# Kernel tuning notes

Hardware: AMD Instinct MI355X
Metric: run time of the kernel (lower is better)

Reference implementation:

```python
import jax, jax.numpy as jnp
import numpy as np

BS, T, N = 16, 50, 100
OBS, ACT, HID, LAT = 40, 8, 64, 16
NEG = -9e15


def _gat(x, adj, w, a_src, a_dst, b, concat, alpha=0.2):
    # x: [B, n, fin]; w: [H, fin, fout]
    h = jnp.einsum('bni,hio->bhno', x, w)
    e_src = jnp.einsum('bhno,ho->bhn', h, a_src[..., 0])
    e_dst = jnp.einsum('bhno,ho->bhn', h, a_dst[..., 0])
    e = e_src[:, :, :, None] + e_dst[:, :, None, :]        # [B,H,n,n]
    e = jnp.where(e > 0, e, alpha * e)                     # LeakyReLU
    e = jnp.where(adj[None, None] > 0, e, NEG)             # mask by adjacency
    att = jax.nn.softmax(e, axis=-1)
    hp = jnp.einsum('bhnm,bhmo->bhno', att, h)
    if concat:
        B, H, n, fo = hp.shape
        return jax.nn.elu(hp.transpose(0, 2, 1, 3).reshape(B, n, H * fo) + b)
    return hp.mean(axis=1) + b


def _lstm(x, Wih, Whh, bih, bhh):
    # x: [B, T, H]; PyTorch gate order i, f, g, o
    def step(carry, xt):
        h, c = carry
        g = xt @ Wih + h @ Whh + bih + bhh
        i, f, gg, o = jnp.split(g, 4, axis=-1)
        c = jax.nn.sigmoid(f) * c + jax.nn.sigmoid(i) * jnp.tanh(gg)
        h = jax.nn.sigmoid(o) * jnp.tanh(c)
        return (h, c), h
    h0 = jnp.zeros((x.shape[0], Whh.shape[0]), x.dtype)
    _, ys = jax.lax.scan(step, (h0, h0), x.transpose(1, 0, 2))
    return ys.transpose(1, 0, 2)


def _forward(o, a_prev, m, eps, params, adj):
    (W_obs, b_obs, W_pa, b_pa, W_mk, b_mk, id_emb,
     lWih, lWhh, lbih, lbhh,
     e1w, e1s, e1d, e1b, e2w, e2s, e2d, e2b,
     d1w, d1s, d1d, d1b, d2w, d2s, d2d, d2b,
     d3w, d3s, d3d, d3b) = params
    bs, t, n, _ = o.shape
    # encode: summed embeddings (dropout is identity in eval)
    emb = (o @ W_obs + b_obs) + (a_prev @ W_pa + b_pa) + (m @ W_mk + b_mk) + id_emb[None, None]
    x = emb.transpose(0, 2, 1, 3).reshape(bs * n, t, HID)
    x = _lstm(x, lWih, lWhh, lbih, lbhh)
    x = x.reshape(bs, n, t, HID).transpose(0, 2, 1, 3).reshape(bs * t, n, HID)
    x = _gat(x, adj, e1w, e1s, e1d, e1b, True)
    x = _gat(x, adj, e2w, e2s, e2d, e2b, False)
    logits = x.reshape(bs, t, n, 2 * LAT).mean(axis=-2)    # AverageGlobalPool over nodes
    mu, logvar = jnp.split(logits, 2, axis=-1)
    z = mu + eps * jnp.exp(0.5 * logvar)                   # reparameterize
    zu = jnp.repeat(z[:, :, None, :], n, axis=2)           # RepeatGlobalUnpool
    d = jnp.concatenate([emb, zu], axis=-1).reshape(bs * t, n, HID + LAT)
    d = _gat(d, adj, d1w, d1s, d1d, d1b, True)
    d = _gat(d, adj, d2w, d2s, d2d, d2b, True)
    d = _gat(d, adj, d3w, d3s, d3d, d3b, False)
    a_recon = d.reshape(bs, t, n, ACT) * m
    return a_recon, mu, logvar


def setup_inputs() -> dict:
    key = jax.random.key(0)
    it = iter(jax.random.split(key, 48))
    def nrm(shape, s=0.1):
        return s * jax.random.normal(next(it), shape, jnp.float32)
    inp = {}
    inp['o'] = jax.random.normal(next(it), (BS, T, N, OBS), jnp.float32)
    inp['a_prev'] = jax.random.uniform(next(it), (BS, T, N, ACT), jnp.float32)
    inp['m'] = (jax.random.uniform(next(it), (BS, T, N, ACT)) > 0.5).astype(jnp.float32)
    inp['eps'] = jax.random.normal(next(it), (BS, T, LAT), jnp.float32)
    adj = jax.random.randint(next(it), (N, N), 0, 2).astype(jnp.int32)
    inp['adj'] = adj.at[jnp.arange(N), jnp.arange(N)].set(1)
    inp['W_obs'] = nrm((OBS, HID)); inp['b_obs'] = jnp.zeros((HID,), jnp.float32)
    inp['W_pa'] = nrm((ACT, HID)); inp['b_pa'] = jnp.zeros((HID,), jnp.float32)
    inp['W_mk'] = nrm((ACT, HID)); inp['b_mk'] = jnp.zeros((HID,), jnp.float32)
    inp['id_emb'] = nrm((N, HID), 1.0)
    inp['lWih'] = nrm((HID, 4 * HID)); inp['lWhh'] = nrm((HID, 4 * HID))
    inp['lbih'] = jnp.zeros((4 * HID,), jnp.float32); inp['lbhh'] = jnp.zeros((4 * HID,), jnp.float32)
    def gat_p(pfx, H, fin, fout, bdim):
        inp[pfx + 'w'] = nrm((H, fin, fout))
        inp[pfx + 's'] = nrm((H, fout, 1))
        inp[pfx + 'd'] = nrm((H, fout, 1))
        inp[pfx + 'b'] = jnp.zeros((bdim,), jnp.float32)
    gat_p('e1', 4, HID, HID // 4, HID)
    gat_p('e2', 1, HID, 2 * LAT, 2 * LAT)
    gat_p('d1', 4, LAT + HID, HID // 4, HID)
    gat_p('d2', 4, HID, HID // 4, HID)
    gat_p('d3', 1, HID, ACT, ACT)
    return inp


def reference(o, a_prev, m, eps, adj, W_obs, b_obs, W_pa, b_pa, W_mk, b_mk, id_emb,
              lWih, lWhh, lbih, lbhh,
              e1w, e1s, e1d, e1b, e2w, e2s, e2d, e2b,
              d1w, d1s, d1d, d1b, d2w, d2s, d2d, d2b,
              d3w, d3s, d3d, d3b):
    params = (W_obs, b_obs, W_pa, b_pa, W_mk, b_mk, id_emb,
              lWih, lWhh, lbih, lbhh,
              e1w, e1s, e1d, e1b, e2w, e2s, e2d, e2b,
              d1w, d1s, d1d, d1b, d2w, d2s, d2d, d2b,
              d3w, d3s, d3d, d3b)
    return _forward(o, a_prev, m, eps, params, adj)
```

## Files before the change

kernel.cpp:

```cpp
#include <hip/hip_runtime.h>

#define BS  16
#define TT  50
#define NN  100
#define OBSF 40
#define ACTF 8
#define HIDF 64
#define LATF 16

typedef __attribute__((ext_vector_type(8))) short bf16x8;
typedef __attribute__((ext_vector_type(4))) float f32x4;
typedef __fp16 f16x2 __attribute__((ext_vector_type(2)));

__device__ __forceinline__ float sigmf(float x) { return 1.f / (1.f + __expf(-x)); }
__device__ __forceinline__ float tanh_fast(float x) { return 1.f - 2.f / (__expf(2.f * x) + 1.f); }
__device__ __forceinline__ short bf16s_rne(float a) {
    unsigned u = __float_as_uint(a); u += 0x7fffu + ((u >> 16) & 1u);
    return (short)(u >> 16);
}
__device__ __forceinline__ unsigned bf16pk_rne(float a, float b) {
    unsigned ua = __float_as_uint(a); ua += 0x7fffu + ((ua >> 16) & 1u);
    unsigned ub = __float_as_uint(b); ub += 0x7fffu + ((ub >> 16) & 1u);
    return (ua >> 16) | (ub & 0xffff0000u);
}

__global__ void adjmask_kernel(const int* __restrict__ adj, unsigned long long* __restrict__ mask) {
    int n = threadIdx.x;
    if (n < NN) {
        unsigned long long w0 = 0ull, w1 = 0ull;
        for (int m = 0; m < 64; ++m)  if (adj[n * NN + m] > 0) w0 |= (1ull << m);
        for (int m = 64; m < NN; ++m) if (adj[n * NN + m] > 0) w1 |= (1ull << (m - 64));
        mask[2 * n] = w0; mask[2 * n + 1] = w1;
    }
}

__global__ void emb_kernel(const float* __restrict__ o, const float* __restrict__ ap,
                           const float* __restrict__ mk,
                           const float* __restrict__ Wobs, const float* __restrict__ bobs,
                           const float* __restrict__ Wpa, const float* __restrict__ bpa,
                           const float* __restrict__ Wmk, const float* __restrict__ bmk,
                           const float* __restrict__ idemb, float* __restrict__ emb) {
    int g = blockIdx.x;
    int n = g % NN;
    int j = threadIdx.x;
    __shared__ float so[OBSF], sa[ACTF], sm[ACTF];
    if (j < OBSF) so[j] = o[(size_t)g * OBSF + j];
    if (j >= 40 && j < 48) sa[j - 40] = ap[(size_t)g * ACTF + (j - 40)];
    if (j >= 48 && j < 56) sm[j - 48] = mk[(size_t)g * ACTF + (j - 48)];
    __syncthreads();
    float acc = bobs[j] + bpa[j] + bmk[j] + idemb[n * HIDF + j];
    #pragma unroll
    for (int k = 0; k < OBSF; ++k) acc += so[k] * Wobs[k * HIDF + j];
    #pragma unroll
    for (int k = 0; k < ACTF; ++k) acc += sa[k] * Wpa[k * HIDF + j] + sm[k] * Wmk[k * HIDF + j];
    emb[(size_t)g * HIDF + j] = acc;
}

__launch_bounds__(256)
__global__ void lstm_mfma_kernel(const float* __restrict__ emb,
                                 const float* __restrict__ Wih, const float* __restrict__ Whh,
                                 const float* __restrict__ bih, const float* __restrict__ bhh,
                                 float* __restrict__ xenc) {
    constexpr int GSTRIDE = 260;
    __shared__ __align__(16) float gbuf[16 * GSTRIDE];
    __shared__ __align__(16) short embt[2][16 * 72];
    __shared__ __align__(16) short hbuf[16 * 72];

    const int tid = threadIdx.x;
    const int wv = tid >> 6, lane = tid & 63, q = lane >> 4, c = lane & 15;

    const int seq = tid >> 4;
    const int part = tid & 15;
    const int s = blockIdx.x * 16 + seq;
    const int b = s / NN, n = s % NN;
    const size_t ebase = ((size_t)b * (TT * NN) + n) * HIDF + part * 4;
    const int u0 = part * 4;
    const size_t xbase = ((size_t)b * (TT * NN) + n) * HIDF + u0;

    union { short s8[8]; bf16x8 v; } bf[2][2][4];
    {
        const int colb = wv * 64 + c;
        #pragma unroll
        for (int m = 0; m < 2; ++m) {
            const float* W = m ? Whh : Wih;
            #pragma unroll
            for (int kc = 0; kc < 2; ++kc)
                #pragma unroll
                for (int nt = 0; nt < 4; ++nt)
                    #pragma unroll
                    for (int j = 0; j < 8; ++j)
                        bf[m][kc][nt].s8[j] = bf16s_rne(W[(size_t)(kc * 32 + q * 8 + j) * 256 + colb + nt * 16]);
        }
    }
    float4 bi, bfo, bg, bo;
    {
        float* bp[4] = {&bi.x, &bfo.x, &bg.x, &bo.x};
        #pragma unroll
        for (int gsel = 0; gsel < 4; ++gsel)
            #pragma unroll
            for (int r = 0; r < 4; ++r)
                bp[gsel][r] = bih[gsel * 64 + u0 + r] + bhh[gsel * 64 + u0 + r];
    }
    for (int i = tid; i < 16 * 72 / 2; i += 256) ((unsigned*)hbuf)[i] = 0u;
    {
        float4 e0 = *(const float4*)&emb[ebase];
        uint2 pk; pk.x = bf16pk_rne(e0.x, e0.y); pk.y = bf16pk_rne(e0.z, e0.w);
        *(uint2*)&embt[0][seq * 72 + part * 4] = pk;
    }
    float cst[4] = {0.f, 0.f, 0.f, 0.f};
    __syncthreads();

    for (int t = 0; t < TT; ++t) {
        float4 pre;
        if (t + 1 < TT) pre = *(const float4*)&emb[ebase + (size_t)(t + 1) * (NN * HIDF)];
        const short* et = &embt[t & 1][0];
        bf16x8 a_e0 = *(const bf16x8*)&et[c * 72 + q * 8];
        bf16x8 a_e1 = *(const bf16x8*)&et[c * 72 + 32 + q * 8];
        bf16x8 a_h0 = *(const bf16x8*)&hbuf[c * 72 + q * 8];
        bf16x8 a_h1 = *(const bf16x8*)&hbuf[c * 72 + 32 + q * 8];
        f32x4 acc[4];
        #pragma unroll
        for (int nt = 0; nt < 4; ++nt) {
            f32x4 a = {0.f, 0.f, 0.f, 0.f};
            a = __builtin_amdgcn_mfma_f32_16x16x32_bf16(a_e0, bf[0][0][nt].v, a, 0, 0, 0);
            a = __builtin_amdgcn_mfma_f32_16x16x32_bf16(a_e1, bf[0][1][nt].v, a, 0, 0, 0);
            a = __builtin_amdgcn_mfma_f32_16x16x32_bf16(a_h0, bf[1][0][nt].v, a, 0, 0, 0);
            a = __builtin_amdgcn_mfma_f32_16x16x32_bf16(a_h1, bf[1][1][nt].v, a, 0, 0, 0);
            acc[nt] = a;
        }
        #pragma unroll
        for (int nt = 0; nt < 4; ++nt)
            #pragma unroll
            for (int r = 0; r < 4; ++r)
                gbuf[(q * 4 + r) * GSTRIDE + wv * 64 + nt * 16 + c] = acc[nt][r];
        __syncthreads();
        if (t + 1 < TT) {
            uint2 pk; pk.x = bf16pk_rne(pre.x, pre.y); pk.y = bf16pk_rne(pre.z, pre.w);
            *(uint2*)&embt[(t + 1) & 1][seq * 72 + part * 4] = pk;
        }
        float4 gi = *(const float4*)&gbuf[seq * GSTRIDE + u0];
        float4 gf = *(const float4*)&gbuf[seq * GSTRIDE + 64 + u0];
        float4 gg = *(const float4*)&gbuf[seq * GSTRIDE + 128 + u0];
        float4 go = *(const float4*)&gbuf[seq * GSTRIDE + 192 + u0];
        float hv[4];
        {
            float gir[4] = {gi.x + bi.x, gi.y + bi.y, gi.z + bi.z, gi.w + bi.w};
            float gfr[4] = {gf.x + bfo.x, gf.y + bfo.y, gf.z + bfo.z, gf.w + bfo.w};
            float ggr[4] = {gg.x + bg.x, gg.y + bg.y, gg.z + bg.z, gg.w + bg.w};
            float gor[4] = {go.x + bo.x, go.y + bo.y, go.z + bo.z, go.w + bo.w};
            #pragma unroll
            for (int r = 0; r < 4; ++r) {
                cst[r] = sigmf(gfr[r]) * cst[r] + sigmf(gir[r]) * tanh_fast(ggr[r]);
                hv[r] = sigmf(gor[r]) * tanh_fast(cst[r]);
            }
        }
        uint2 hpk; hpk.x = bf16pk_rne(hv[0], hv[1]); hpk.y = bf16pk_rne(hv[2], hv[3]);
        *(uint2*)&hbuf[seq * 72 + u0] = hpk;
        float4 xo; xo.x = hv[0]; xo.y = hv[1]; xo.z = hv[2]; xo.w = hv[3];
        *(float4*)&xenc[xbase + (size_t)t * (NN * HIDF)] = xo;
        __syncthreads();
    }
}

template <int FIN1, int FIN2, int H, int FOUT, int SPLIT, int OUTMODE>
__launch_bounds__(256)
__global__ void gat_kernel(const float* __restrict__ x1, const float* __restrict__ x2,
                           const float* __restrict__ w, const float* __restrict__ asrc,
                           const float* __restrict__ adst, const float* __restrict__ bias,
                           const unsigned long long* __restrict__ adjmask,
                           const float* __restrict__ mgate, float* __restrict__ out) {
    constexpr int FIN = FIN1 + FIN2;
    constexpr int HF = H * FOUT;
    constexpr int NPT = 256 / HF;
    constexpr int ROWS = (NN + NPT - 1) / NPT;
    constexpr int SXB = NN * FIN1 * 4;
    constexpr int SHB = HF * 112 * 2;
    constexpr int R1 = (SXB > SHB) ? SXB : SHB;
    __shared__ __align__(16) char smem[R1];
    float* sx = (float*)smem;
    __fp16* sh16 = (__fp16*)smem;
    __shared__ float sz[FIN2 > 0 ? FIN2 : 1];
    __shared__ __align__(16) float ses[H * 112];
    __shared__ __align__(16) float sed[H * 112];
    __shared__ unsigned long long smask[2 * NN];
    int g = blockIdx.x;
    int tid = threadIdx.x;

    for (int i = tid; i < NN * FIN1; i += 256) {
        int n = i / FIN1, k = i % FIN1;
        sx[n * FIN1 + k] = x1[((size_t)g * NN + n) * FIN1 + k];
    }
    if constexpr (FIN2 > 0) {
        if (tid < FIN2) sz[tid] = x2[(size_t)g * FIN2 + tid];
    }
    if (tid < 2 * NN) smask[tid] = adjmask[tid];
    __syncthreads();

    const int ho = tid % HF;
    const int h = ho / FOUT, o = ho % FOUT;
    const int n0 = tid / HF;
    float racc[ROWS];
    {
        float wcol[FIN];
        #pragma unroll
        for (int k = 0; k < FIN; ++k) wcol[k] = w[((size_t)h * FIN + k) * FOUT + o];
        float zdot = 0.f;
        if constexpr (FIN2 > 0) {
            #pragma unroll
            for (int k = 0; k < FIN2; ++k) zdot += sz[k] * wcol[FIN1 + k];
        }
        const float as = asrc[ho], ad = adst[ho];
        #pragma unroll
        for (int r = 0; r < ROWS; ++r) {
            int n = n0 + r * NPT;
            float acc = zdot;
            if (ROWS * NPT == NN || n < NN) {
                const float4* row = (const float4*)&sx[n * FIN1];
                #pragma unroll
                for (int k4 = 0; k4 < FIN1 / 4; ++k4) {
                    float4 xv = row[k4];
                    acc += xv.x * wcol[4 * k4] + xv.y * wcol[4 * k4 + 1]
                         + xv.z * wcol[4 * k4 + 2] + xv.w * wcol[4 * k4 + 3];
                }
            }
            racc[r] = acc;
            float vs = acc * as, vd = acc * ad;
            #pragma unroll
            for (int off = FOUT / 2; off >= 1; off >>= 1) {
                vs += __shfl_xor(vs, off, 64);
                vd += __shfl_xor(vd, off, 64);
            }
            if (o == 0 && (ROWS * NPT == NN || n < NN)) {
                ses[h * 112 + n] = vs; sed[h * 112 + n] = vd;
            }
        }
    }
    __syncthreads();
    #pragma unroll
    for (int r = 0; r < ROWS; ++r) {
        int n = n0 + r * NPT;
        if (ROWS * NPT == NN || n < NN) sh16[ho * 112 + n] = (__fp16)racc[r];
    }
    for (int i = tid; i < HF * 12; i += 256)
        sh16[(i / 12) * 112 + 100 + (i % 12)] = (__fp16)0.f;
    for (int i = tid; i < H * 12; i += 256)
        sed[(i / 12) * 112 + 100 + (i % 12)] = 0.f;
    __syncthreads();

    constexpr int FT = FOUT / SPLIT;
    constexpr int ITEMS = H * NN * SPLIT;
    for (int idx = tid; idx < ITEMS; idx += 256) {
        int h2 = idx / (NN * SPLIT);
        int rem = idx % (NN * SPLIT);
        int n = rem / SPLIT;
        int os = (rem % SPLIT) * FT;
        unsigned long long m0 = smask[2 * n], m1 = smask[2 * n + 1];
        float esn = ses[h2 * 112 + n];
        float denom = 0.f;
        float acc[FT];
        #pragma unroll
        for (int qq = 0; qq < FT; ++qq) acc[qq] = 0.f;
        const float4* sedf4 = (const float4*)&sed[h2 * 112];
        const __fp16* hb = &sh16[(h2 * FOUT + os) * 112];
        #pragma unroll 2
        for (int gg = 0; gg < 13; ++gg) {
            unsigned mb = (gg < 8) ? (unsigned)(m0 >> (8 * gg)) & 0xffu
                                   : (unsigned)(m1 >> (8 * (gg - 8))) & 0xffu;
            float4 edA = sedf4[2 * gg];
            float4 edB = sedf4[2 * gg + 1];
            float e0 = esn + edA.x; e0 = fmaxf(e0, 0.2f * e0);
            float e1 = esn + edA.y; e1 = fmaxf(e1, 0.2f * e1);
            float e2 = esn + edA.z; e2 = fmaxf(e2, 0.2f * e2);
            float e3 = esn + edA.w; e3 = fmaxf(e3, 0.2f * e3);
            float e4 = esn + edB.x; e4 = fmaxf(e4, 0.2f * e4);
            float e5 = esn + edB.y; e5 = fmaxf(e5, 0.2f * e5);
            float e6 = esn + edB.z; e6 = fmaxf(e6, 0.2f * e6);
            float e7 = esn + edB.w; e7 = fmaxf(e7, 0.2f * e7);
            float p0 = (mb & 1u)   ? __expf(e0) : 0.f;
            float p1 = (mb & 2u)   ? __expf(e1) : 0.f;
            float p2 = (mb & 4u)   ? __expf(e2) : 0.f;
            float p3 = (mb & 8u)   ? __expf(e3) : 0.f;
            float p4 = (mb & 16u)  ? __expf(e4) : 0.f;
            float p5 = (mb & 32u)  ? __expf(e5) : 0.f;
            float p6 = (mb & 64u)  ? __expf(e6) : 0.f;
            float p7 = (mb & 128u) ? __expf(e7) : 0.f;
            denom += ((p0 + p1) + (p2 + p3)) + ((p4 + p5) + (p6 + p7));
            f16x2 q01 = __builtin_amdgcn_cvt_pkrtz(p0, p1);
            f16x2 q23 = __builtin_amdgcn_cvt_pkrtz(p2, p3);
            f16x2 q45 = __builtin_amdgcn_cvt_pkrtz(p4, p5);
            f16x2 q67 = __builtin_amdgcn_cvt_pkrtz(p6, p7);
            #pragma unroll
            for (int oo = 0; oo < FT; ++oo) {
                const f16x2* hp = (const f16x2*)&hb[oo * 112 + gg * 8];
                float a = acc[oo];
                a = __builtin_amdgcn_fdot2(q01, hp[0], a, false);
                a = __builtin_amdgcn_fdot2(q23, hp[1], a, false);
                a = __builtin_amdgcn_fdot2(q45, hp[2], a, false);
                a = __builtin_amdgcn_fdot2(q67, hp[3], a, false);
                acc[oo] = a;
            }
        }
        float inv = 1.f / denom;
        if constexpr (OUTMODE == 0) {
            float4* op = (float4*)&out[((size_t)g * NN + n) * HF + h2 * FOUT + os];
            #pragma unroll
            for (int q4 = 0; q4 < FT / 4; ++q4) {
                float4 v;
                float a0 = acc[4 * q4 + 0] * inv + bias[h2 * FOUT + os + 4 * q4 + 0];
                float a1 = acc[4 * q4 + 1] * inv + bias[h2 * FOUT + os + 4 * q4 + 1];
                float a2 = acc[4 * q4 + 2] * inv + bias[h2 * FOUT + os + 4 * q4 + 2];
                float a3 = acc[4 * q4 + 3] * inv + bias[h2 * FOUT + os + 4 * q4 + 3];
                v.x = (a0 > 0.f) ? a0 : (__expf(a0) - 1.f);
                v.y = (a1 > 0.f) ? a1 : (__expf(a1) - 1.f);
                v.z = (a2 > 0.f) ? a2 : (__expf(a2) - 1.f);
                v.w = (a3 > 0.f) ? a3 : (__expf(a3) - 1.f);
                op[q4] = v;
            }
        } else if constexpr (OUTMODE == 1) {
            float4* op = (float4*)&out[((size_t)g * NN + n) * FOUT + os];
            #pragma unroll
            for (int q4 = 0; q4 < FT / 4; ++q4) {
                float4 v;
                v.x = acc[4 * q4 + 0] * inv + bias[os + 4 * q4 + 0];
                v.y = acc[4 * q4 + 1] * inv + bias[os + 4 * q4 + 1];
                v.z = acc[4 * q4 + 2] * inv + bias[os + 4 * q4 + 2];
                v.w = acc[4 * q4 + 3] * inv + bias[os + 4 * q4 + 3];
                op[q4] = v;
            }
        } else {
            size_t base = ((size_t)g * NN + n) * FOUT + os;
            float4* op = (float4*)&out[base];
            const float4* mp = (const float4*)&mgate[base];
            #pragma unroll
            for (int q4 = 0; q4 < FT / 4; ++q4) {
                float4 mv = mp[q4];
                float4 v;
                v.x = (acc[4 * q4 + 0] * inv + bias[os + 4 * q4 + 0]) * mv.x;
                v.y = (acc[4 * q4 + 1] * inv + bias[os + 4 * q4 + 1]) * mv.y;
                v.z = (acc[4 * q4 + 2] * inv + bias[os + 4 * q4 + 2]) * mv.z;
                v.w = (acc[4 * q4 + 3] * inv + bias[os + 4 * q4 + 3]) * mv.w;
                op[q4] = v;
            }
        }
    }
}

__global__ void pool_kernel(const float* __restrict__ g2, const float* __restrict__ eps,
                            float* __restrict__ z, float* __restrict__ dout) {
    int g = blockIdx.x;
    int c = threadIdx.x;
    __shared__ float s[2 * LATF];
    if (c < 2 * LATF) {
        float sum = 0.f;
        for (int n = 0; n < NN; ++n) sum += g2[((size_t)g * NN + n) * (2 * LATF) + c];
        s[c] = sum * (1.f / NN);
    }
    __syncthreads();
    if (c < LATF) {
        float mu = s[c], lv = s[LATF + c];
        dout[640000 + (size_t)g * LATF + c] = mu;
        dout[652800 + (size_t)g * LATF + c] = lv;
        z[(size_t)g * LATF + c] = mu + eps[(size_t)g * LATF + c] * __expf(0.5f * lv);
    }
}

extern "C" void kernel_launch(void* const* d_in, const int* in_sizes, int n_in,
                              void* d_out, int out_size, void* d_ws, size_t ws_size,
                              hipStream_t stream) {
    const float* o     = (const float*)d_in[0];
    const float* aprev = (const float*)d_in[1];
    const float* mk    = (const float*)d_in[2];
    const float* eps   = (const float*)d_in[3];
    const int*   adj   = (const int*)d_in[4];
    const float* Wobs  = (const float*)d_in[5];
    const float* bobs  = (const float*)d_in[6];
    const float* Wpa   = (const float*)d_in[7];
    const float* bpa   = (const float*)d_in[8];
    const float* Wmk   = (const float*)d_in[9];
    const float* bmk   = (const float*)d_in[10];
    const float* idemb = (const float*)d_in[11];
    const float* lWih  = (const float*)d_in[12];
    const float* lWhh  = (const float*)d_in[13];
    const float* lbih  = (const float*)d_in[14];
    const float* lbhh  = (const float*)d_in[15];
    const float* e1w = (const float*)d_in[16]; const float* e1s = (const float*)d_in[17];
    const float* e1d = (const float*)d_in[18]; const float* e1b = (const float*)d_in[19];
    const float* e2w = (const float*)d_in[20]; const float* e2s = (const float*)d_in[21];
    const float* e2d = (const float*)d_in[22]; const float* e2b = (const float*)d_in[23];
    const float* d1w = (const float*)d_in[24]; const float* d1s = (const float*)d_in[25];
    const float* d1d = (const float*)d_in[26]; const float* d1b = (const float*)d_in[27];
    const float* d2w = (const float*)d_in[28]; const float* d2s = (const float*)d_in[29];
    const float* d2d = (const float*)d_in[30]; const float* d2b = (const float*)d_in[31];
    const float* d3w = (const float*)d_in[32]; const float* d3s = (const float*)d_in[33];
    const float* d3d = (const float*)d_in[34]; const float* d3b = (const float*)d_in[35];

    float* ws   = (float*)d_ws;
    float* emb  = ws;
    float* xenc = ws + 5120000;
    float* g1o  = ws + 10240000;
    float* g2o  = ws + 15360000;
    float* z    = ws + 17920000;
    float* d1o  = ws + 18000000;
    float* d2o  = ws + 23200000;
    unsigned long long* amask = (unsigned long long*)(ws + 30720000);
    float* out = (float*)d_out;

    adjmask_kernel<<<1, 128, 0, stream>>>(adj, amask);
    emb_kernel<<<BS * TT * NN, 64, 0, stream>>>(o, aprev, mk, Wobs, bobs, Wpa, bpa,
                                                Wmk, bmk, idemb, emb);
    lstm_mfma_kernel<<<100, 256, 0, stream>>>(emb, lWih, lWhh, lbih, lbhh, xenc);
    gat_kernel<64, 0, 4, 16, 1, 0><<<800, 256, 0, stream>>>(xenc, nullptr, e1w, e1s, e1d, e1b,
                                                            amask, nullptr, g1o);
    gat_kernel<64, 0, 1, 32, 4, 1><<<800, 256, 0, stream>>>(g1o, nullptr, e2w, e2s, e2d, e2b,
                                                            amask, nullptr, g2o);
    pool_kernel<<<800, 64, 0, stream>>>(g2o, eps, z, out);
    gat_kernel<64, 16, 4, 16, 1, 0><<<800, 256, 0, stream>>>(emb, z, d1w, d1s, d1d, d1b,
                                                             amask, nullptr, d1o);
    gat_kernel<64, 0, 4, 16, 1, 0><<<800, 256, 0, stream>>>(d1o, nullptr, d2w, d2s, d2d, d2b,
                                                            amask, nullptr, d2o);
    gat_kernel<64, 0, 1, 8, 2, 2><<<800, 256, 0, stream>>>(d2o, nullptr, d3w, d3s, d3d, d3b,
                                                           amask, mk, out);
}
```

Baseline: 526.3 us.

## Use bf16 MFMA for 4-head GAT projection and attention-score computation

Adds a specialized gat4h_kernel for the three 4-head GAT layers. It converts node features and weights to bf16 in shared memory and computes the projection with MFMA 16x16x32 instructions. The attention source and destination scores come from a second MFMA against precomputed W·a vectors, which replaces the per-thread scalar dot products and shuffle reductions. The fp16 H buffer stride also changes from 112 to 120. This trades fp32 precision for bf16 in the projection inputs and adds per-block weight preprocessing.

```diff
diff --git a/kernel.cpp b/kernel.cpp
--- a/kernel.cpp
+++ b/kernel.cpp
@@ -162,106 +162,141 @@
     }
 }
 
-template <int FIN1, int FIN2, int H, int FOUT, int SPLIT, int OUTMODE>
+template <int FIN2>
 __launch_bounds__(256)
-__global__ void gat_kernel(const float* __restrict__ x1, const float* __restrict__ x2,
-                           const float* __restrict__ w, const float* __restrict__ asrc,
-                           const float* __restrict__ adst, const float* __restrict__ bias,
-                           const unsigned long long* __restrict__ adjmask,
-                           const float* __restrict__ mgate, float* __restrict__ out) {
-    constexpr int FIN = FIN1 + FIN2;
-    constexpr int HF = H * FOUT;
-    constexpr int NPT = 256 / HF;
-    constexpr int ROWS = (NN + NPT - 1) / NPT;
-    constexpr int SXB = NN * FIN1 * 4;
-    constexpr int SHB = HF * 112 * 2;
-    constexpr int R1 = (SXB > SHB) ? SXB : SHB;
-    __shared__ __align__(16) char smem[R1];
-    float* sx = (float*)smem;
-    __fp16* sh16 = (__fp16*)smem;
-    __shared__ float sz[FIN2 > 0 ? FIN2 : 1];
-    __shared__ __align__(16) float ses[H * 112];
-    __shared__ __align__(16) float sed[H * 112];
+__global__ void gat4h_kernel(const float* __restrict__ x1, const float* __restrict__ x2,
+                             const float* __restrict__ w, const float* __restrict__ asrc,
+                             const float* __restrict__ adst, const float* __restrict__ bias,
+                             const unsigned long long* __restrict__ adjmask,
+                             float* __restrict__ out) {
+    constexpr int FIN = 64 + FIN2;
+    __shared__ __align__(16) char regA[112 * 72 * 2];
+    __shared__ __align__(16) short swb[64 * 72];
+    __shared__ __align__(16) short wab[16 * 72];
+    __shared__ __align__(16) float ses[4 * 112];
+    __shared__ __align__(16) float sed[4 * 112];
+    __shared__ float szd[64];
+    __shared__ float sesc[4], sedc[4];
     __shared__ unsigned long long smask[2 * NN];
-    int g = blockIdx.x;
-    int tid = threadIdx.x;
-
-    for (int i = tid; i < NN * FIN1; i += 256) {
-        int n = i / FIN1, k = i % FIN1;
-        sx[n * FIN1 + k] = x1[((size_t)g * NN + n) * FIN1 + k];
+    short* sxa = (short*)regA;
+    __fp16* sh16 = (__fp16*)regA;
+
+    const int g = blockIdx.x, tid = threadIdx.x;
+    const int wv = tid >> 6, lane = tid & 63, q = lane >> 4, c = lane & 15;
+
+    for (int i = tid; i < 112 * 36; i += 256) {
+        int n = i / 36, k2 = i % 36, k = 2 * k2;
+        float lo = 0.f, hi = 0.f;
+        if (n < NN && k < 64) {
+            float2 v = *(const float2*)&x1[((size_t)g * NN + n) * 64 + k];
+            lo = v.x; hi = v.y;
+        }
+        ((unsigned*)sxa)[i] = bf16pk_rne(lo, hi);
+    }
+    for (int i = tid; i < 64 * 36; i += 256) {
+        int nc = i / 36, k2 = i % 36, k = 2 * k2;
+        int h = nc >> 4, o = nc & 15;
+        float lo = 0.f, hi = 0.f;
+        if (k < 64) {
+            lo = w[((size_t)h * FIN + k) * 16 + o];
+            hi = w[((size_t)h * FIN + k + 1) * 16 + o];
+        }
+        ((unsigned*)swb)[i] = bf16pk_rne(lo, hi);
+    }
+    for (int i = tid; i < 16 * 36; i += 256) {
+        int col = i / 36, k2 = i % 36, k = 2 * k2;
+        float lo = 0.f, hi = 0.f;
+        if (col < 8 && k < 64) {
+            int h = col >> 1;
+            const float* av = (col & 1) ? adst : asrc;
+            float s0 = 0.f, s1 = 0.f;
+            #pragma unroll
+            for (int o = 0; o < 16; ++o) {
+                float a = av[h * 16 + o];
+                s0 += w[((size_t)h * FIN + k) * 16 + o] * a;
+                s1 += w[((size_t)h * FIN + k + 1) * 16 + o] * a;
+            }
+            lo = s0; hi = s1;
+        }
+        ((unsigned*)wab)[i] = bf16pk_rne(lo, hi);
     }
     if constexpr (FIN2 > 0) {
-        if (tid < FIN2) sz[tid] = x2[(size_t)g * FIN2 + tid];
+        if (tid < 64) {
+            int h = tid >> 4, o = tid & 15;
+            float s = 0.f;
+            #pragma unroll
+            for (int k = 0; k < FIN2; ++k)
+                s += x2[(size_t)g * FIN2 + k] * w[((size_t)h * FIN + 64 + k) * 16 + o];
+            szd[tid] = s;
+        }
     }
     if (tid < 2 * NN) smask[tid] = adjmask[tid];
     __syncthreads();
 
-    const int ho = tid % HF;
-    const int h = ho / FOUT, o = ho % FOUT;
-    const int n0 = tid / HF;
-    float racc[ROWS];
-    {
-        float wcol[FIN];
-        #pragma unroll
-        for (int k = 0; k < FIN; ++k) wcol[k] = w[((size_t)h * FIN + k) * FOUT + o];
-        float zdot = 0.f;
-        if constexpr (FIN2 > 0) {
-            #pragma unroll
-            for (int k = 0; k < FIN2; ++k) zdot += sz[k] * wcol[FIN1 + k];
-        }
-        const float as = asrc[ho], ad = adst[ho];
-        #pragma unroll
-        for (int r = 0; r < ROWS; ++r) {
-            int n = n0 + r * NPT;
-            float acc = zdot;
-            if (ROWS * NPT == NN || n < NN) {
-                const float4* row = (const float4*)&sx[n * FIN1];
-                #pragma unroll
-                for (int k4 = 0; k4 < FIN1 / 4; ++k4) {
-                    float4 xv = row[k4];
-                    acc += xv.x * wcol[4 * k4] + xv.y * wcol[4 * k4 + 1]
-                         + xv.z * wcol[4 * k4 + 2] + xv.w * wcol[4 * k4 + 3];
-                }
-            }
-            racc[r] = acc;
-            float vs = acc * as, vd = acc * ad;
-            #pragma unroll
-            for (int off = FOUT / 2; off >= 1; off >>= 1) {
-                vs += __shfl_xor(vs, off, 64);
-                vd += __shfl_xor(vd, off, 64);
-            }
-            if (o == 0 && (ROWS * NPT == NN || n < NN)) {
-                ses[h * 112 + n] = vs; sed[h * 112 + n] = vd;
-            }
-        }
-    }
-    __syncthreads();
+    if constexpr (FIN2 > 0) {
+        if (tid < 8) {
+            int h = tid >> 1;
+            const float* av = (tid & 1) ? adst : asrc;
+            float s = 0.f;
+            #pragma unroll
+            for (int o = 0; o < 16; ++o) s += szd[h * 16 + o] * av[h * 16 + o];
+            if (tid & 1) sedc[h] = s; else sesc[h] = s;
+        }
+    }
+
+    f32x4 hc[7], ec[7];
     #pragma unroll
-    for (int r = 0; r < ROWS; ++r) {
-        int n = n0 + r * NPT;
-        if (ROWS * NPT == NN || n < NN) sh16[ho * 112 + n] = (__fp16)racc[r];
-    }
-    for (int i = tid; i < HF * 12; i += 256)
-        sh16[(i / 12) * 112 + 100 + (i % 12)] = (__fp16)0.f;
-    for (int i = tid; i < H * 12; i += 256)
-        sed[(i / 12) * 112 + 100 + (i % 12)] = 0.f;
-    __syncthreads();
-
-    constexpr int FT = FOUT / SPLIT;
-    constexpr int ITEMS = H * NN * SPLIT;
-    for (int idx = tid; idx < ITEMS; idx += 256) {
-        int h2 = idx / (NN * SPLIT);
-        int rem = idx % (NN * SPLIT);
-        int n = rem / SPLIT;
-        int os = (rem % SPLIT) * FT;
+    for (int mt = 0; mt < 7; ++mt) {
+        hc[mt] = f32x4{0.f, 0.f, 0.f, 0.f};
+        ec[mt] = f32x4{0.f, 0.f, 0.f, 0.f};
+    }
+    #pragma unroll
+    for (int kc = 0; kc < 2; ++kc) {
+        bf16x8 bfr = *(const bf16x8*)&swb[(wv * 16 + c) * 72 + kc * 32 + q * 8];
+        bf16x8 wfr = *(const bf16x8*)&wab[c * 72 + kc * 32 + q * 8];
+        #pragma unroll
+        for (int mt = 0; mt < 7; ++mt) {
+            bf16x8 afr = *(const bf16x8*)&sxa[(mt * 16 + c) * 72 + kc * 32 + q * 8];
+            hc[mt] = __builtin_amdgcn_mfma_f32_16x16x32_bf16(afr, bfr, hc[mt], 0, 0, 0);
+            ec[mt] = __builtin_amdgcn_mfma_f32_16x16x32_bf16(afr, wfr, ec[mt], 0, 0, 0);
+        }
+    }
+    float zdv = 0.f, escv = 0.f, edcv = 0.f;
+    if constexpr (FIN2 > 0) {
+        zdv = szd[wv * 16 + c];
+        escv = sesc[wv]; edcv = sedc[wv];
+    }
+    __syncthreads();
+
+    #pragma unroll
+    for (int mt = 0; mt < 7; ++mt) {
+        f16x2 p01, p23;
+        p01[0] = (__fp16)(hc[mt][0] + zdv); p01[1] = (__fp16)(hc[mt][1] + zdv);
+        p23[0] = (__fp16)(hc[mt][2] + zdv); p23[1] = (__fp16)(hc[mt][3] + zdv);
+        f16x2* dst = (f16x2*)&sh16[(wv * 16 + c) * 120 + mt * 16 + q * 4];
+        dst[0] = p01; dst[1] = p23;
+        int nb = wv * 112 + mt * 16 + q * 4;
+        if (c == 2 * wv) {
+            ses[nb + 0] = ec[mt][0] + escv; ses[nb + 1] = ec[mt][1] + escv;
+            ses[nb + 2] = ec[mt][2] + escv; ses[nb + 3] = ec[mt][3] + escv;
+        } else if (c == 2 * wv + 1) {
+            sed[nb + 0] = ec[mt][0] + edcv; sed[nb + 1] = ec[mt][1] + edcv;
+            sed[nb + 2] = ec[mt][2] + edcv; sed[nb + 3] = ec[mt][3] + edcv;
+        }
+    }
+    __syncthreads();
+
+    for (int idx = tid; idx < 4 * NN; idx += 256) {
+        int h2 = idx / NN;
+        int n = idx % NN;
         unsigned long long m0 = smask[2 * n], m1 = smask[2 * n + 1];
         float esn = ses[h2 * 112 + n];
         float denom = 0.f;
-        float acc[FT];
-        #pragma unroll
-        for (int qq = 0; qq < FT; ++qq) acc[qq] = 0.f;
+        float acc[16];
+        #pragma unroll
+        for (int qq = 0; qq < 16; ++qq) acc[qq] = 0.f;
         const float4* sedf4 = (const float4*)&sed[h2 * 112];
-        const __fp16* hb = &sh16[(h2 * FOUT + os) * 112];
+        const __fp16* hb = &sh16[(h2 * 16) * 120];
         #pragma unroll 2
         for (int gg = 0; gg < 13; ++gg) {
             unsigned mb = (gg < 8) ? (unsigned)(m0 >> (8 * gg)) & 0xffu
@@ -290,8 +325,8 @@
             f16x2 q45 = __builtin_amdgcn_cvt_pkrtz(p4, p5);
             f16x2 q67 = __builtin_amdgcn_cvt_pkrtz(p6, p7);
             #pragma unroll
-            for (int oo = 0; oo < FT; ++oo) {
-                const f16x2* hp = (const f16x2*)&hb[oo * 112 + gg * 8];
+            for (int oo = 0; oo < 16; ++oo) {
+                const f16x2* hp = (const f16x2*)&hb[oo * 120 + gg * 8];
                 float a = acc[oo];
                 a = __builtin_amdgcn_fdot2(q01, hp[0], a, false);
                 a = __builtin_amdgcn_fdot2(q23, hp[1], a, false);
@@ -301,22 +336,163 @@
             }
         }
         float inv = 1.f / denom;
-        if constexpr (OUTMODE == 0) {
-            float4* op = (float4*)&out[((size_t)g * NN + n) * HF + h2 * FOUT + os];
-            #pragma unroll
-            for (int q4 = 0; q4 < FT / 4; ++q4) {
-                float4 v;
-                float a0 = acc[4 * q4 + 0] * inv + bias[h2 * FOUT + os + 4 * q4 + 0];
-                float a1 = acc[4 * q4 + 1] * inv + bias[h2 * FOUT + os + 4 * q4 + 1];
-                float a2 = acc[4 * q4 + 2] * inv + bias[h2 * FOUT + os + 4 * q4 + 2];
-                float a3 = acc[4 * q4 + 3] * inv + bias[h2 * FOUT + os + 4 * q4 + 3];
-                v.x = (a0 > 0.f) ? a0 : (__expf(a0) - 1.f);
-                v.y = (a1 > 0.f) ? a1 : (__expf(a1) - 1.f);
-                v.z = (a2 > 0.f) ? a2 : (__expf(a2) - 1.f);
-                v.w = (a3 > 0.f) ? a3 : (__expf(a3) - 1.f);
-                op[q4] = v;
-            }
-        } else if constexpr (OUTMODE == 1) {
+        float4* op = (float4*)&out[((size_t)g * NN + n) * 64 + h2 * 16];
+        #pragma unroll
+        for (int q4 = 0; q4 < 4; ++q4) {
+            float4 v;
+            float a0 = acc[4 * q4 + 0] * inv + bias[h2 * 16 + 4 * q4 + 0];
+            float a1 = acc[4 * q4 + 1] * inv + bias[h2 * 16 + 4 * q4 + 1];
+            float a2 = acc[4 * q4 + 2] * inv + bias[h2 * 16 + 4 * q4 + 2];
+            float a3 = acc[4 * q4 + 3] * inv + bias[h2 * 16 + 4 * q4 + 3];
+            v.x = (a0 > 0.f) ? a0 : (__expf(a0) - 1.f);
+            v.y = (a1 > 0.f) ? a1 : (__expf(a1) - 1.f);
+            v.z = (a2 > 0.f) ? a2 : (__expf(a2) - 1.f);
+            v.w = (a3 > 0.f) ? a3 : (__expf(a3) - 1.f);
+            op[q4] = v;
+        }
+    }
+}
+
+template <int FIN1, int FIN2, int H, int FOUT, int SPLIT, int OUTMODE>
+__launch_bounds__(256)
+__global__ void gat_kernel(const float* __restrict__ x1, const float* __restrict__ x2,
+                           const float* __restrict__ w, const float* __restrict__ asrc,
+                           const float* __restrict__ adst, const float* __restrict__ bias,
+                           const unsigned long long* __restrict__ adjmask,
+                           const float* __restrict__ mgate, float* __restrict__ out) {
+    constexpr int FIN = FIN1 + FIN2;
+    constexpr int HF = H * FOUT;
+    constexpr int NPT = 256 / HF;
+    constexpr int ROWS = (NN + NPT - 1) / NPT;
+    constexpr int SXB = NN * FIN1 * 4;
+    constexpr int SHB = HF * 120 * 2;
+    constexpr int R1 = (SXB > SHB) ? SXB : SHB;
+    __shared__ __align__(16) char smem[R1];
+    float* sx = (float*)smem;
+    __fp16* sh16 = (__fp16*)smem;
+    __shared__ float sz[FIN2 > 0 ? FIN2 : 1];
+    __shared__ __align__(16) float ses[H * 112];
+    __shared__ __align__(16) float sed[H * 112];
+    __shared__ unsigned long long smask[2 * NN];
+    int g = blockIdx.x;
+    int tid = threadIdx.x;
+
+    for (int i = tid; i < NN * FIN1; i += 256) {
+        int n = i / FIN1, k = i % FIN1;
+        sx[n * FIN1 + k] = x1[((size_t)g * NN + n) * FIN1 + k];
+    }
+    if constexpr (FIN2 > 0) {
+        if (tid < FIN2) sz[tid] = x2[(size_t)g * FIN2 + tid];
+    }
+    if (tid < 2 * NN) smask[tid] = adjmask[tid];
+    __syncthreads();
+
+    const int ho = tid % HF;
+    const int h = ho / FOUT, o = ho % FOUT;
+    const int n0 = tid / HF;
+    float racc[ROWS];
+    {
+        float wcol[FIN];
+        #pragma unroll
+        for (int k = 0; k < FIN; ++k) wcol[k] = w[((size_t)h * FIN + k) * FOUT + o];
+        float zdot = 0.f;
+        if constexpr (FIN2 > 0) {
+            #pragma unroll
+            for (int k = 0; k < FIN2; ++k) zdot += sz[k] * wcol[FIN1 + k];
+        }
+        const float as = asrc[ho], ad = adst[ho];
+        #pragma unroll
+        for (int r = 0; r < ROWS; ++r) {
+            int n = n0 + r * NPT;
+            float acc = zdot;
+            if (ROWS * NPT == NN || n < NN) {
+                const float4* row = (const float4*)&sx[n * FIN1];
+                #pragma unroll
+                for (int k4 = 0; k4 < FIN1 / 4; ++k4) {
+                    float4 xv = row[k4];
+                    acc += xv.x * wcol[4 * k4] + xv.y * wcol[4 * k4 + 1]
+                         + xv.z * wcol[4 * k4 + 2] + xv.w * wcol[4 * k4 + 3];
+                }
+            }
+            racc[r] = acc;
+            float vs = acc * as, vd = acc * ad;
+            #pragma unroll
+            for (int off = FOUT / 2; off >= 1; off >>= 1) {
+                vs += __shfl_xor(vs, off, 64);
+                vd += __shfl_xor(vd, off, 64);
+            }
+            if (o == 0 && (ROWS * NPT == NN || n < NN)) {
+                ses[h * 112 + n] = vs; sed[h * 112 + n] = vd;
+            }
+        }
+    }
+    __syncthreads();
+    #pragma unroll
+    for (int r = 0; r < ROWS; ++r) {
+        int n = n0 + r * NPT;
+        if (ROWS * NPT == NN || n < NN) sh16[ho * 120 + n] = (__fp16)racc[r];
+    }
+    for (int i = tid; i < HF * 20; i += 256)
+        sh16[(i / 20) * 120 + 100 + (i % 20)] = (__fp16)0.f;
+    for (int i = tid; i < H * 12; i += 256)
+        sed[(i / 12) * 112 + 100 + (i % 12)] = 0.f;
+    __syncthreads();
+
+    constexpr int FT = FOUT / SPLIT;
+    constexpr int ITEMS = H * NN * SPLIT;
+    for (int idx = tid; idx < ITEMS; idx += 256) {
+        int h2 = idx / (NN * SPLIT);
+        int rem = idx % (NN * SPLIT);
+        int n = rem / SPLIT;
+        int os = (rem % SPLIT) * FT;
+        unsigned long long m0 = smask[2 * n], m1 = smask[2 * n + 1];
+        float esn = ses[h2 * 112 + n];
+        float denom = 0.f;
+        float acc[FT];
+        #pragma unroll
+        for (int qq = 0; qq < FT; ++qq) acc[qq] = 0.f;
+        const float4* sedf4 = (const float4*)&sed[h2 * 112];
+        const __fp16* hb = &sh16[(h2 * FOUT + os) * 120];
+        #pragma unroll 2
+        for (int gg = 0; gg < 13; ++gg) {
+            unsigned mb = (gg < 8) ? (unsigned)(m0 >> (8 * gg)) & 0xffu
+                                   : (unsigned)(m1 >> (8 * (gg - 8))) & 0xffu;
+            float4 edA = sedf4[2 * gg];
+            float4 edB = sedf4[2 * gg + 1];
+            float e0 = esn + edA.x; e0 = fmaxf(e0, 0.2f * e0);
+            float e1 = esn + edA.y; e1 = fmaxf(e1, 0.2f * e1);
+            float e2 = esn + edA.z; e2 = fmaxf(e2, 0.2f * e2);
+            float e3 = esn + edA.w; e3 = fmaxf(e3, 0.2f * e3);
+            float e4 = esn + edB.x; e4 = fmaxf(e4, 0.2f * e4);
+            float e5 = esn + edB.y; e5 = fmaxf(e5, 0.2f * e5);
+            float e6 = esn + edB.z; e6 = fmaxf(e6, 0.2f * e6);
+            float e7 = esn + edB.w; e7 = fmaxf(e7, 0.2f * e7);
+            float p0 = (mb & 1u)   ? __expf(e0) : 0.f;
+            float p1 = (mb & 2u)   ? __expf(e1) : 0.f;
+            float p2 = (mb & 4u)   ? __expf(e2) : 0.f;
+            float p3 = (mb & 8u)   ? __expf(e3) : 0.f;
+            float p4 = (mb & 16u)  ? __expf(e4) : 0.f;
+            float p5 = (mb & 32u)  ? __expf(e5) : 0.f;
+            float p6 = (mb & 64u)  ? __expf(e6) : 0.f;
+            float p7 = (mb & 128u) ? __expf(e7) : 0.f;
+            denom += ((p0 + p1) + (p2 + p3)) + ((p4 + p5) + (p6 + p7));
+            f16x2 q01 = __builtin_amdgcn_cvt_pkrtz(p0, p1);
+            f16x2 q23 = __builtin_amdgcn_cvt_pkrtz(p2, p3);
+            f16x2 q45 = __builtin_amdgcn_cvt_pkrtz(p4, p5);
+            f16x2 q67 = __builtin_amdgcn_cvt_pkrtz(p6, p7);
+            #pragma unroll
+            for (int oo = 0; oo < FT; ++oo) {
+                const f16x2* hp = (const f16x2*)&hb[oo * 120 + gg * 8];
+                float a = acc[oo];
+                a = __builtin_amdgcn_fdot2(q01, hp[0], a, false);
+                a = __builtin_amdgcn_fdot2(q23, hp[1], a, false);
+                a = __builtin_amdgcn_fdot2(q45, hp[2], a, false);
+                a = __builtin_amdgcn_fdot2(q67, hp[3], a, false);
+                acc[oo] = a;
+            }
+        }
+        float inv = 1.f / denom;
+        if constexpr (OUTMODE == 1) {
             float4* op = (float4*)&out[((size_t)g * NN + n) * FOUT + os];
             #pragma unroll
             for (int q4 = 0; q4 < FT / 4; ++q4) {
@@ -409,15 +585,12 @@
     emb_kernel<<<BS * TT * NN, 64, 0, stream>>>(o, aprev, mk, Wobs, bobs, Wpa, bpa,
                                                 Wmk, bmk, idemb, emb);
     lstm_mfma_kernel<<<100, 256, 0, stream>>>(emb, lWih, lWhh, lbih, lbhh, xenc);
-    gat_kernel<64, 0, 4, 16, 1, 0><<<800, 256, 0, stream>>>(xenc, nullptr, e1w, e1s, e1d, e1b,
-                                                            amask, nullptr, g1o);
+    gat4h_kernel<0><<<800, 256, 0, stream>>>(xenc, nullptr, e1w, e1s, e1d, e1b, amask, g1o);
     gat_kernel<64, 0, 1, 32, 4, 1><<<800, 256, 0, stream>>>(g1o, nullptr, e2w, e2s, e2d, e2b,
                                                             amask, nullptr, g2o);
     pool_kernel<<<800, 64, 0, stream>>>(g2o, eps, z, out);
-    gat_kernel<64, 16, 4, 16, 1, 0><<<800, 256, 0, stream>>>(emb, z, d1w, d1s, d1d, d1b,
-                                                             amask, nullptr, d1o);
-    gat_kernel<64, 0, 4, 16, 1, 0><<<800, 256, 0, stream>>>(d1o, nullptr, d2w, d2s, d2d, d2b,
-                                                            amask, nullptr, d2o);
+    gat4h_kernel<16><<<800, 256, 0, stream>>>(emb, z, d1w, d1s, d1d, d1b, amask, d1o);
+    gat4h_kernel<0><<<800, 256, 0, stream>>>(d1o, nullptr, d2w, d2s, d2d, d2b, amask, d2o);
     gat_kernel<64, 0, 1, 8, 2, 2><<<800, 256, 0, stream>>>(d2o, nullptr, d3w, d3s, d3d, d3b,
                                                            amask, mk, out);
 }
```

New measurement: 480.5 us. 8.7% less time.
